# Optimization experiments

Measured on AMD Instinct MI355X. Metric: run time of the kernel, lower is better.

The kernel has to match this reference:

```python
import jax, jax.numpy as jnp
import numpy as np

PATCH = 32          # feature map is PATCH x PATCH, N = PATCH**2 tokens
HEADS = 8
HD = 24             # head_dim (hardcoded in Block -> Cluster3D)
P = 4               # proposal_w = proposal_h = 4 -> 16 cluster centers
EPS_NORM = 1e-12    # F.normalize eps
LN_EPS = 1e-5


def _layernorm(x, g, b):
    m = x.mean(-1, keepdims=True)
    v = ((x - m) ** 2).mean(-1, keepdims=True)
    return (x - m) / jnp.sqrt(v + LN_EPS) * g + b


def _cluster3d(xn, f_w, f_b, v_w, v_b, alpha, beta, proj_w, proj_b):
    # xn: [B, N, D] with tokens laid out row-major over a PATCH x PATCH grid
    B, N, D = xn.shape
    M = P * P
    feat = xn @ f_w.T + f_b   # [B, N, HEADS*HD]  (1x1 conv f)
    val = xn @ v_w.T + v_b    # [B, N, HEADS*HD]  (1x1 conv v)

    def to_heads(t):  # channel layout is (e c): head-major
        return t.reshape(B, N, HEADS, HD).transpose(0, 2, 1, 3).reshape(B * HEADS, N, HD)

    fh = to_heads(feat)       # [Bh, N, HD]
    vh = to_heads(val)

    def pool(t):  # AdaptiveAvgPool to (P, P) over the PATCH x PATCH grid
        g = t.reshape(-1, P, PATCH // P, P, PATCH // P, HD).mean(axis=(2, 4))
        return g.reshape(-1, M, HD)

    centers = pool(fh)        # [Bh, M, HD]
    vcenters = pool(vh)       # [Bh, M, HD]

    cn = centers / jnp.clip(jnp.linalg.norm(centers, axis=-1, keepdims=True), EPS_NORM)
    fn = fh / jnp.clip(jnp.linalg.norm(fh, axis=-1, keepdims=True), EPS_NORM)
    sim = beta + alpha * jnp.einsum('bmc,bnc->bmn', cn, fn)   # [Bh, M, N]
    sim = jnp.where(sim >= 0, sim, 0.2 * sim)                 # LeakyReLU(0.2); dropout eval=identity

    # hard top-1 assignment of each token to its best center
    idx = jnp.argmax(sim, axis=1)                              # [Bh, N]
    mask = jax.nn.one_hot(idx, M, dtype=sim.dtype).transpose(0, 2, 1)  # [Bh, M, N]
    mask = jax.lax.stop_gradient(mask)
    sim = sim * mask

    # aggregate tokens into centers, then dispatch back
    agg = (jnp.einsum('bmn,bnc->bmc', sim, vh) + vcenters) / (mask.sum(-1, keepdims=True) + 1.0)
    out = jnp.einsum('bmn,bmc->bnc', sim, agg)                 # [Bh, N, HD]

    out = out.reshape(B, HEADS, N, HD).transpose(0, 2, 1, 3).reshape(B, N, HEADS * HD)
    return out @ proj_w.T + proj_b                             # [B, N, D]


def setup_inputs() -> dict:
    key = jax.random.key(0)
    ks = jax.random.split(key, 8)
    B, N, D, HID, HH = 64, PATCH * PATCH, 512, 2048, HEADS * HD
    s = 0.02
    return {
        'x': jax.random.normal(ks[0], (B, N, D), jnp.float32),
        'ln1_g': jnp.ones((D,), jnp.float32),
        'ln1_b': jnp.zeros((D,), jnp.float32),
        'f_w': jax.random.normal(ks[1], (HH, D), jnp.float32) * s,
        'f_b': jnp.zeros((HH,), jnp.float32),
        'v_w': jax.random.normal(ks[2], (HH, D), jnp.float32) * s,
        'v_b': jnp.zeros((HH,), jnp.float32),
        'sim_alpha': jnp.ones((1,), jnp.float32),
        'sim_beta': jnp.zeros((1,), jnp.float32),
        'proj_w': jax.random.normal(ks[3], (D, HH), jnp.float32) * s,
        'proj_b': jnp.zeros((D,), jnp.float32),
        'ln2_g': jnp.ones((D,), jnp.float32),
        'ln2_b': jnp.zeros((D,), jnp.float32),
        'fc1_w': jax.random.normal(ks[4], (HID, D), jnp.float32) * s,
        'fc1_b': jnp.zeros((HID,), jnp.float32),
        'fc2_w': jax.random.normal(ks[5], (D, HID), jnp.float32) * s,
        'fc2_b': jnp.zeros((D,), jnp.float32),
    }


def reference(x, ln1_g, ln1_b, f_w, f_b, v_w, v_b, sim_alpha, sim_beta,
              proj_w, proj_b, ln2_g, ln2_b, fc1_w, fc1_b, fc2_w, fc2_b):
    x = x + _cluster3d(_layernorm(x, ln1_g, ln1_b), f_w, f_b, v_w, v_b,
                       sim_alpha, sim_beta, proj_w, proj_b)
    h = _layernorm(x, ln2_g, ln2_b)
    h = jax.nn.gelu(h @ fc1_w.T + fc1_b, approximate=False)
    x = x + (h @ fc2_w.T + fc2_b)
    return x
```

## Files before the change

### kernel.cpp

```cpp
#include <hip/hip_runtime.h>


typedef __attribute__((ext_vector_type(8))) short short8;
typedef __attribute__((ext_vector_type(4))) short short4v;
typedef __attribute__((ext_vector_type(4))) float floatx4;

static __device__ __forceinline__ short f2bf(float f) {
  union { float f; unsigned u; } a; a.f = f;
  unsigned r = a.u + 0x7fffu + ((a.u >> 16) & 1u);
  return (short)(r >> 16);
}

static __device__ __forceinline__ void gload_lds16(const short* g, short* l) {
  __builtin_amdgcn_global_load_lds(
      (const __attribute__((address_space(1))) void*)g,
      (__attribute__((address_space(3))) void*)l, 16, 0, 0);
}

__global__ __launch_bounds__(256) void cvt_f32_bf16(
    const float* __restrict__ in, short* __restrict__ out, int n4)
{
  int i = blockIdx.x * 256 + threadIdx.x;
  if (i >= n4) return;
  float4 v = reinterpret_cast<const float4*>(in)[i];
  short4v o;
  o[0] = f2bf(v.x); o[1] = f2bf(v.y); o[2] = f2bf(v.z); o[3] = f2bf(v.w);
  reinterpret_cast<short4v*>(out)[i] = o;
}

__global__ __launch_bounds__(256) void ln_kernel(
    const float* __restrict__ x, const float* __restrict__ g,
    const float* __restrict__ b, short* __restrict__ out)
{
  const int wave = threadIdx.x >> 6, lane = threadIdx.x & 63;
  const size_t row = (size_t)blockIdx.x * 4 + wave;
  const float* xr = x + row * 512;
  const int c = lane * 8;
  float4 v0 = *reinterpret_cast<const float4*>(xr + c);
  float4 v1 = *reinterpret_cast<const float4*>(xr + c + 4);
  float xs[8] = {v0.x, v0.y, v0.z, v0.w, v1.x, v1.y, v1.z, v1.w};
  float s = 0.f, q = 0.f;
#pragma unroll
  for (int k = 0; k < 8; ++k) { s += xs[k]; q += xs[k] * xs[k]; }
#pragma unroll
  for (int off = 32; off; off >>= 1) {
    s += __shfl_xor(s, off);
    q += __shfl_xor(q, off);
  }
  const float mean = s * (1.0f / 512.0f);
  const float var  = q * (1.0f / 512.0f) - mean * mean;
  const float rstd = rsqrtf(var + 1e-5f);
  short8 o;
#pragma unroll
  for (int k = 0; k < 8; ++k)
    o[k] = f2bf((xs[k] - mean) * rstd * g[c + k] + b[c + k]);
  *reinterpret_cast<short8*>(out + row * 512 + c) = o;
}

template<int BM, int BN, int WM, int WN, int EPI>
__global__ __launch_bounds__(256, 2) void gemm_bt(
    const short* __restrict__ A, const short* __restrict__ W,
    const float* __restrict__ bias, const float* __restrict__ resid,
    float* __restrict__ Cf, short* __restrict__ Cb,
    const int N, const int K)
{
  constexpr int BK = 32;
  constexpr int T  = 256;
  constexpr int AC = (BM * BK / 8) / T;
  constexpr int WC = (BN * BK / 8) / T;
  __shared__ short Al[2][BM * BK];
  __shared__ short Wl[2][BN * BK];
  const int tid  = threadIdx.x;
  const int wave = tid >> 6;
  const int lane = tid & 63;
  constexpr int WCOLS = BN / WN;
  const int wm = (wave / WCOLS) * WM;
  const int wn = (wave % WCOLS) * WN;
  constexpr int MI = WM / 16, NJ = WN / 16;
  const int row0 = blockIdx.x * BM;
  const int col0 = blockIdx.y * BN;
  const int r  = lane & 15;
  const int kc = lane >> 4;

  floatx4 acc[MI][NJ];
#pragma unroll
  for (int i = 0; i < MI; ++i)
#pragma unroll
    for (int j = 0; j < NJ; ++j)
      acc[i][j] = (floatx4){0.f, 0.f, 0.f, 0.f};

  const short* Ab = A + (size_t)row0 * K;
  const short* Wb = W + (size_t)col0 * K;

  const short* aSrc[AC]; int aDst[AC];
#pragma unroll
  for (int u = 0; u < AC; ++u) {
    const int cc = u * T + tid;
    const int rr = cc >> 2, sl = cc & 3;
    const int co = sl ^ ((rr >> 1) & 3);
    aSrc[u] = Ab + (size_t)rr * K + co * 8;
    aDst[u] = cc * 8;
  }
  const short* wSrc[WC]; int wDst[WC];
#pragma unroll
  for (int u = 0; u < WC; ++u) {
    const int cc = u * T + tid;
    const int rr = cc >> 2, sl = cc & 3;
    const int co = sl ^ ((rr >> 1) & 3);
    wSrc[u] = Wb + (size_t)rr * K + co * 8;
    wDst[u] = cc * 8;
  }
  int aOff[MI], wOff[NJ];
#pragma unroll
  for (int i = 0; i < MI; ++i) {
    const int rt = wm + 16 * i + r;
    aOff[i] = rt * BK + ((kc ^ ((rt >> 1) & 3)) << 3);
  }
#pragma unroll
  for (int j = 0; j < NJ; ++j) {
    const int rt = wn + 16 * j + r;
    wOff[j] = rt * BK + ((kc ^ ((rt >> 1) & 3)) << 3);
  }

  auto stage = [&](int buf, int k0) {
#pragma unroll
    for (int u = 0; u < AC; ++u) gload_lds16(aSrc[u] + k0, &Al[buf][aDst[u]]);
#pragma unroll
    for (int u = 0; u < WC; ++u) gload_lds16(wSrc[u] + k0, &Wl[buf][wDst[u]]);
  };

  stage(0, 0);
  __syncthreads();
  int cur = 0;
  for (int k0 = BK; k0 <= K; k0 += BK) {
    if (k0 < K) stage(cur ^ 1, k0);
    short8 af[MI], wfr[NJ];
#pragma unroll
    for (int i = 0; i < MI; ++i)
      af[i] = *reinterpret_cast<const short8*>(&Al[cur][aOff[i]]);
#pragma unroll
    for (int j = 0; j < NJ; ++j)
      wfr[j] = *reinterpret_cast<const short8*>(&Wl[cur][wOff[j]]);
#pragma unroll
    for (int i = 0; i < MI; ++i)
#pragma unroll
      for (int j = 0; j < NJ; ++j)
        acc[i][j] = __builtin_amdgcn_mfma_f32_16x16x32_bf16(
            af[i], wfr[j], acc[i][j], 0, 0, 0);
    __syncthreads();
    cur ^= 1;
  }

#pragma unroll
  for (int i = 0; i < MI; ++i) {
#pragma unroll
    for (int j = 0; j < NJ; ++j) {
      const int col = col0 + wn + 16 * j + r;
      const float bv = bias[col];
#pragma unroll
      for (int t = 0; t < 4; ++t) {
        const int rowi = row0 + wm + 16 * i + (lane >> 4) * 4 + t;
        const size_t offo = (size_t)rowi * N + col;
        float v = acc[i][j][t] + bv;
        if (EPI == 0) {
          Cf[offo] = v;
        } else if (EPI == 1) {
          Cf[offo] = v + resid[offo];
        } else {
          v = 0.5f * v * (1.0f + erff(v * 0.70710678118654752f));
          Cb[offo] = f2bf(v);
        }
      }
    }
  }
}

template<int EPI>
__global__ __launch_bounds__(512, 1) void gemm512(
    const short* __restrict__ A, const short* __restrict__ W,
    const float* __restrict__ bias, const float* __restrict__ resid,
    float* __restrict__ Cf, short* __restrict__ Cb,
    const int N, const int K)
{
  constexpr int BM = 256, BN = 256, BK = 32;
  constexpr int T  = 512;
  constexpr int AC = (BM * BK / 8) / T;
  constexpr int WC = (BN * BK / 8) / T;
  constexpr int WM = 128, WN = 64;
  constexpr int MI = WM / 16, NJ = WN / 16;
  __shared__ short Al[2][BM * BK];
  __shared__ short Wl[2][BN * BK];
  const int tid  = threadIdx.x;
  const int wave = tid >> 6;
  const int lane = tid & 63;
  const int wm = (wave >> 2) * WM;
  const int wn = (wave & 3) * WN;
  const int row0 = blockIdx.x * BM;
  const int col0 = blockIdx.y * BN;
  const int r  = lane & 15;
  const int kc = lane >> 4;

  floatx4 acc[MI][NJ];
#pragma unroll
  for (int i = 0; i < MI; ++i)
#pragma unroll
    for (int j = 0; j < NJ; ++j)
      acc[i][j] = (floatx4){0.f, 0.f, 0.f, 0.f};

  const short* Ab = A + (size_t)row0 * K;
  const short* Wb = W + (size_t)col0 * K;

  const short* aSrc[AC]; int aDst[AC];
#pragma unroll
  for (int u = 0; u < AC; ++u) {
    const int cc = u * T + tid;
    const int rr = cc >> 2, sl = cc & 3;
    const int co = sl ^ ((rr >> 1) & 3);
    aSrc[u] = Ab + (size_t)rr * K + co * 8;
    aDst[u] = cc * 8;
  }
  const short* wSrc[WC]; int wDst[WC];
#pragma unroll
  for (int u = 0; u < WC; ++u) {
    const int cc = u * T + tid;
    const int rr = cc >> 2, sl = cc & 3;
    const int co = sl ^ ((rr >> 1) & 3);
    wSrc[u] = Wb + (size_t)rr * K + co * 8;
    wDst[u] = cc * 8;
  }
  int aOff[MI], wOff[NJ];
#pragma unroll
  for (int i = 0; i < MI; ++i) {
    const int rt = wm + 16 * i + r;
    aOff[i] = rt * BK + ((kc ^ ((rt >> 1) & 3)) << 3);
  }
#pragma unroll
  for (int j = 0; j < NJ; ++j) {
    const int rt = wn + 16 * j + r;
    wOff[j] = rt * BK + ((kc ^ ((rt >> 1) & 3)) << 3);
  }

  auto stage = [&](int buf, int k0) {
#pragma unroll
    for (int u = 0; u < AC; ++u) gload_lds16(aSrc[u] + k0, &Al[buf][aDst[u]]);
#pragma unroll
    for (int u = 0; u < WC; ++u) gload_lds16(wSrc[u] + k0, &Wl[buf][wDst[u]]);
  };

  stage(0, 0);
  __syncthreads();
  int cur = 0;
  for (int k0 = BK; k0 <= K; k0 += BK) {
    if (k0 < K) stage(cur ^ 1, k0);
    short8 af[MI], wfr[NJ];
#pragma unroll
    for (int i = 0; i < MI; ++i)
      af[i] = *reinterpret_cast<const short8*>(&Al[cur][aOff[i]]);
#pragma unroll
    for (int j = 0; j < NJ; ++j)
      wfr[j] = *reinterpret_cast<const short8*>(&Wl[cur][wOff[j]]);
#pragma unroll
    for (int i = 0; i < MI; ++i)
#pragma unroll
      for (int j = 0; j < NJ; ++j)
        acc[i][j] = __builtin_amdgcn_mfma_f32_16x16x32_bf16(
            af[i], wfr[j], acc[i][j], 0, 0, 0);
    __syncthreads();
    cur ^= 1;
  }

#pragma unroll
  for (int i = 0; i < MI; ++i) {
#pragma unroll
    for (int j = 0; j < NJ; ++j) {
      const int col = col0 + wn + 16 * j + r;
      const float bv = bias[col];
#pragma unroll
      for (int t = 0; t < 4; ++t) {
        const int rowi = row0 + wm + 16 * i + kc * 4 + t;
        const size_t offo = (size_t)rowi * N + col;
        float v = acc[i][j][t] + bv;
        if (EPI == 1) {
          Cf[offo] = v + resid[offo];
        } else {
          v = 0.5f * v * (1.0f + erff(v * 0.70710678118654752f));
          Cb[offo] = f2bf(v);
        }
      }
    }
  }
}

__global__ __launch_bounds__(384) void pool_kernel(
    const float* __restrict__ feat, const float* __restrict__ val,
    float* __restrict__ cn, float* __restrict__ vcent)
{
  const int bh = blockIdx.x;
  const int b = bh >> 3, h = bh & 7;
  const int t = threadIdx.x;
  const int m = t / 24, c = t % 24;
  const int cy = m >> 2, cx = m & 3;
  const size_t base = (size_t)b * 1024 * 192 + h * 24 + c;
  float sf = 0.f, sv = 0.f;
  for (int dy = 0; dy < 8; ++dy) {
    const int ny = (cy * 8 + dy) * 32 + cx * 8;
    for (int dx = 0; dx < 8; ++dx) {
      const size_t off = base + (size_t)(ny + dx) * 192;
      sf += feat[off];
      sv += val[off];
    }
  }
  sf *= (1.0f / 64.0f); sv *= (1.0f / 64.0f);
  __shared__ float cent[16][24];
  cent[m][c] = sf;
  vcent[(size_t)bh * 384 + t] = sv;
  __syncthreads();
  float nrm = 0.f;
#pragma unroll
  for (int k = 0; k < 24; ++k) nrm += cent[m][k] * cent[m][k];
  nrm = fmaxf(sqrtf(nrm), 1e-12f);
  cn[(size_t)bh * 384 + t] = sf / nrm;
}

__global__ __launch_bounds__(256) void sim_kernel(
    const float* __restrict__ feat, const float* __restrict__ cn,
    const float* __restrict__ alpha_p, const float* __restrict__ beta_p,
    float* __restrict__ sval, int* __restrict__ sidx)
{
  const int bh = blockIdx.y;
  const int b = bh >> 3, h = bh & 7;
  __shared__ float cs[384];
  for (int i = threadIdx.x; i < 384; i += 256) cs[i] = cn[(size_t)bh * 384 + i];
  __syncthreads();
  const int n = blockIdx.x * 256 + threadIdx.x;
  const float* f = feat + (size_t)(b * 1024 + n) * 192 + h * 24;
  float v[24];
#pragma unroll
  for (int k = 0; k < 24; k += 4) {
    float4 t4 = *reinterpret_cast<const float4*>(f + k);
    v[k] = t4.x; v[k + 1] = t4.y; v[k + 2] = t4.z; v[k + 3] = t4.w;
  }
  float q = 0.f;
#pragma unroll
  for (int k = 0; k < 24; ++k) q += v[k] * v[k];
  const float inv = 1.0f / fmaxf(sqrtf(q), 1e-12f);
  const float alpha = alpha_p[0], beta = beta_p[0];
  float best = -3.4e38f; int bi = 0;
#pragma unroll
  for (int m = 0; m < 16; ++m) {
    float d = 0.f;
#pragma unroll
    for (int k = 0; k < 24; ++k) d += cs[m * 24 + k] * v[k];
    float s = beta + alpha * (d * inv);
    s = (s < 0.f) ? 0.2f * s : s;
    if (s > best) { best = s; bi = m; }
  }
  sval[(size_t)bh * 1024 + n] = best;
  sidx[(size_t)bh * 1024 + n] = bi;
}

__global__ __launch_bounds__(256) void agg_kernel(
    const float* __restrict__ val, const float* __restrict__ vcent,
    const float* __restrict__ sval, const int* __restrict__ sidx,
    float* __restrict__ agg)
{
  const int bh = blockIdx.x;
  const int b = bh >> 3, h = bh & 7;
  __shared__ float acc[384];
  __shared__ float cnt[16];
  for (int i = threadIdx.x; i < 384; i += 256) acc[i] = 0.f;
  if (threadIdx.x < 16) cnt[threadIdx.x] = 0.f;
  __syncthreads();
  for (int n = threadIdx.x; n < 1024; n += 256) {
    const float s = sval[(size_t)bh * 1024 + n];
    const int m = sidx[(size_t)bh * 1024 + n];
    atomicAdd(&cnt[m], 1.0f);
    const float* vv = val + (size_t)(b * 1024 + n) * 192 + h * 24;
#pragma unroll
    for (int k = 0; k < 24; ++k) atomicAdd(&acc[m * 24 + k], s * vv[k]);
  }
  __syncthreads();
  for (int i = threadIdx.x; i < 384; i += 256) {
    const int m = i / 24;
    agg[(size_t)bh * 384 + i] = (acc[i] + vcent[(size_t)bh * 384 + i]) / (cnt[m] + 1.0f);
  }
}

__global__ __launch_bounds__(256) void dispatch_kernel(
    const float* __restrict__ sval, const int* __restrict__ sidx,
    const float* __restrict__ agg, short* __restrict__ o)
{
  const int g = blockIdx.x * 256 + threadIdx.x;
  const int h = g & 7, n = (g >> 3) & 1023, b = g >> 13;
  const int bh = b * 8 + h;
  const float s = sval[(size_t)bh * 1024 + n];
  const int m = sidx[(size_t)bh * 1024 + n];
  const float* a = agg + (size_t)bh * 384 + m * 24;
  short* op = o + ((size_t)(b * 1024 + n)) * 192 + h * 24;
  short8 pack[3];
#pragma unroll
  for (int k = 0; k < 24; ++k) pack[k >> 3][k & 7] = f2bf(s * a[k]);
  short8* dst = reinterpret_cast<short8*>(op);
  dst[0] = pack[0]; dst[1] = pack[1]; dst[2] = pack[2];
}

extern "C" void kernel_launch(void* const* d_in, const int* in_sizes, int n_in,
                              void* d_out, int out_size, void* d_ws, size_t ws_size,
                              hipStream_t stream)
{
  const float* x      = (const float*)d_in[0];
  const float* ln1_g  = (const float*)d_in[1];
  const float* ln1_b  = (const float*)d_in[2];
  const float* f_w    = (const float*)d_in[3];
  const float* f_b    = (const float*)d_in[4];
  const float* v_w    = (const float*)d_in[5];
  const float* v_b    = (const float*)d_in[6];
  const float* alpha  = (const float*)d_in[7];
  const float* beta   = (const float*)d_in[8];
  const float* proj_w = (const float*)d_in[9];
  const float* proj_b = (const float*)d_in[10];
  const float* ln2_g  = (const float*)d_in[11];
  const float* ln2_b  = (const float*)d_in[12];
  const float* fc1_w  = (const float*)d_in[13];
  const float* fc1_b  = (const float*)d_in[14];
  const float* fc2_w  = (const float*)d_in[15];
  const float* fc2_b  = (const float*)d_in[16];
  float* out = (float*)d_out;

  char* ws = (char*)d_ws;
  size_t off = 0;
  auto alloc = [&](size_t bytes) -> char* {
    char* p = ws + off;
    off = (off + bytes + 255) & ~(size_t)255;
    return p;
  };
  short* xn   = (short*)alloc(67108864);
  float* feat = (float*)alloc(50331648);
  float* val  = (float*)alloc(50331648);
  short* o    = (short*)alloc(25165824);
  float* x1   = (float*)alloc(134217728);
  short* wf   = (short*)alloc(196608);
  short* wv   = (short*)alloc(196608);
  short* wp   = (short*)alloc(196608);
  short* w1   = (short*)alloc(2097152);
  short* w2   = (short*)alloc(2097152);
  float* cnb  = (float*)alloc(786432);
  float* vcb  = (float*)alloc(786432);
  float* agb  = (float*)alloc(786432);
  float* svb  = (float*)alloc(2097152);
  int*   sib  = (int*)  alloc(2097152);
  short* h  = (short*)feat;

  const size_t h1_bytes = 134217728;
  short* h1;
  int nchunk;
  if (ws_size >= off + h1_bytes) {
    h1 = (short*)alloc(h1_bytes);
    nchunk = 2;
  } else {
    h1 = xn;
    nchunk = 4;
  }
  const int MCH = 65536 / nchunk;

  cvt_f32_bf16<<<96,   256, 0, stream>>>(f_w,    wf, 24576);
  cvt_f32_bf16<<<96,   256, 0, stream>>>(v_w,    wv, 24576);
  cvt_f32_bf16<<<96,   256, 0, stream>>>(proj_w, wp, 24576);
  cvt_f32_bf16<<<1024, 256, 0, stream>>>(fc1_w,  w1, 262144);
  cvt_f32_bf16<<<1024, 256, 0, stream>>>(fc2_w,  w2, 262144);

  ln_kernel<<<16384, 256, 0, stream>>>(x, ln1_g, ln1_b, xn);

  gemm_bt<256, 64, 64, 64, 0><<<dim3(256, 3), 256, 0, stream>>>(
      xn, wf, f_b, nullptr, feat, nullptr, 192, 512);
  gemm_bt<256, 64, 64, 64, 0><<<dim3(256, 3), 256, 0, stream>>>(
      xn, wv, v_b, nullptr, val, nullptr, 192, 512);

  pool_kernel<<<512, 384, 0, stream>>>(feat, val, cnb, vcb);
  sim_kernel<<<dim3(4, 512), 256, 0, stream>>>(feat, cnb, alpha, beta, svb, sib);
  agg_kernel<<<512, 256, 0, stream>>>(val, vcb, svb, sib, agb);
  dispatch_kernel<<<2048, 256, 0, stream>>>(svb, sib, agb, o);

  gemm_bt<128, 128, 64, 64, 1><<<dim3(512, 4), 256, 0, stream>>>(
      o, wp, proj_b, x, x1, nullptr, 512, 192);

  ln_kernel<<<16384, 256, 0, stream>>>(x1, ln2_g, ln2_b, h);

  for (int c = 0; c < nchunk; ++c) {
    const short* hA = h + (size_t)c * MCH * 512;
    gemm512<2><<<dim3(MCH / 256, 8), 512, 0, stream>>>(
        hA, w1, fc1_b, nullptr, nullptr, h1, 2048, 512);
    gemm512<1><<<dim3(MCH / 256, 2), 512, 0, stream>>>(
        h1, w2, fc2_b, x1 + (size_t)c * MCH * 512,
        out + (size_t)c * MCH * 512, nullptr, 512, 2048);
  }
  (void)in_sizes; (void)n_in; (void)out_size;
}
```

Before: 1.184 ms.

## Retune MLP GEMMs for occupancy, fast GELU, and fewer chunks

The MLP GEMM kernel goes from a double-buffered LDS pipeline to a single buffer with launch bounds allowing several blocks per CU. The fc2 GEMM uses a narrower 128-column tile so it launches more blocks. Exact erff is replaced with an Abramowitz-Stegun polynomial erf approximation in the GELU epilogues, and a single-chunk path is added when the workspace is large enough. The aim is more latency hiding through occupancy and cheaper epilogue math, at the cost of giving up load/compute overlap inside a block and a small loss of GELU accuracy.

```diff
diff --git a/kernel.cpp b/kernel.cpp
--- a/kernel.cpp
+++ b/kernel.cpp
@@ -9,6 +9,20 @@
   union { float f; unsigned u; } a; a.f = f;
   unsigned r = a.u + 0x7fffu + ((a.u >> 16) & 1u);
   return (short)(r >> 16);
+}
+
+static __device__ __forceinline__ float gelu_fast(float v) {
+  const float xs = v * 0.70710678118654752f;
+  const float ax = fabsf(xs);
+  const float t  = __frcp_rn(fmaf(0.3275911f, ax, 1.0f));
+  float p = fmaf(t, 1.061405429f, -1.453152027f);
+  p = fmaf(t, p, 1.421413741f);
+  p = fmaf(t, p, -0.284496736f);
+  p = fmaf(t, p, 0.254829592f);
+  p = p * t;
+  const float er = 1.0f - p * __expf(-ax * ax);
+  const float e  = (xs < 0.f) ? -er : er;
+  return 0.5f * v * (1.0f + e);
 }
 
 static __device__ __forceinline__ void gload_lds16(const short* g, short* l) {
@@ -167,36 +181,36 @@
         } else if (EPI == 1) {
           Cf[offo] = v + resid[offo];
         } else {
-          v = 0.5f * v * (1.0f + erff(v * 0.70710678118654752f));
-          Cb[offo] = f2bf(v);
+          Cb[offo] = f2bf(gelu_fast(v));
         }
       }
     }
   }
 }
 
-template<int EPI>
-__global__ __launch_bounds__(512, 1) void gemm512(
+template<int BN_, int WROWS, int EPI>
+__global__ __launch_bounds__(512, 4) void gemm512s(
     const short* __restrict__ A, const short* __restrict__ W,
     const float* __restrict__ bias, const float* __restrict__ resid,
     float* __restrict__ Cf, short* __restrict__ Cb,
     const int N, const int K)
 {
-  constexpr int BM = 256, BN = 256, BK = 32;
+  constexpr int BM = 256, BK = 32;
   constexpr int T  = 512;
   constexpr int AC = (BM * BK / 8) / T;
-  constexpr int WC = (BN * BK / 8) / T;
-  constexpr int WM = 128, WN = 64;
+  constexpr int WC = (BN_ * BK / 8) / T;
+  constexpr int WCOLS = 8 / WROWS;
+  constexpr int WM = BM / WROWS, WN = BN_ / WCOLS;
   constexpr int MI = WM / 16, NJ = WN / 16;
-  __shared__ short Al[2][BM * BK];
-  __shared__ short Wl[2][BN * BK];
+  __shared__ short Al[BM * BK];
+  __shared__ short Wl[BN_ * BK];
   const int tid  = threadIdx.x;
   const int wave = tid >> 6;
   const int lane = tid & 63;
-  const int wm = (wave >> 2) * WM;
-  const int wn = (wave & 3) * WN;
+  const int wm = (wave / WCOLS) * WM;
+  const int wn = (wave % WCOLS) * WN;
   const int row0 = blockIdx.x * BM;
-  const int col0 = blockIdx.y * BN;
+  const int col0 = blockIdx.y * BN_;
   const int r  = lane & 15;
   const int kc = lane >> 4;
 
@@ -240,33 +254,26 @@
     wOff[j] = rt * BK + ((kc ^ ((rt >> 1) & 3)) << 3);
   }
 
-  auto stage = [&](int buf, int k0) {
-#pragma unroll
-    for (int u = 0; u < AC; ++u) gload_lds16(aSrc[u] + k0, &Al[buf][aDst[u]]);
-#pragma unroll
-    for (int u = 0; u < WC; ++u) gload_lds16(wSrc[u] + k0, &Wl[buf][wDst[u]]);
-  };
-
-  stage(0, 0);
-  __syncthreads();
-  int cur = 0;
-  for (int k0 = BK; k0 <= K; k0 += BK) {
-    if (k0 < K) stage(cur ^ 1, k0);
-    short8 af[MI], wfr[NJ];
+  for (int k0 = 0; k0 < K; k0 += BK) {
+#pragma unroll
+    for (int u = 0; u < AC; ++u) gload_lds16(aSrc[u] + k0, &Al[aDst[u]]);
+#pragma unroll
+    for (int u = 0; u < WC; ++u) gload_lds16(wSrc[u] + k0, &Wl[wDst[u]]);
+    __syncthreads();
+    short8 af[MI], wf[NJ];
 #pragma unroll
     for (int i = 0; i < MI; ++i)
-      af[i] = *reinterpret_cast<const short8*>(&Al[cur][aOff[i]]);
+      af[i] = *reinterpret_cast<const short8*>(&Al[aOff[i]]);
 #pragma unroll
     for (int j = 0; j < NJ; ++j)
-      wfr[j] = *reinterpret_cast<const short8*>(&Wl[cur][wOff[j]]);
+      wf[j] = *reinterpret_cast<const short8*>(&Wl[wOff[j]]);
 #pragma unroll
     for (int i = 0; i < MI; ++i)
 #pragma unroll
       for (int j = 0; j < NJ; ++j)
         acc[i][j] = __builtin_amdgcn_mfma_f32_16x16x32_bf16(
-            af[i], wfr[j], acc[i][j], 0, 0, 0);
+            af[i], wf[j], acc[i][j], 0, 0, 0);
     __syncthreads();
-    cur ^= 1;
   }
 
 #pragma unroll
@@ -276,15 +283,14 @@
       const int col = col0 + wn + 16 * j + r;
       const float bv = bias[col];
 #pragma unroll
-      for (int t = 0; t < 4; ++t) {
-        const int rowi = row0 + wm + 16 * i + kc * 4 + t;
+      for (int tt = 0; tt < 4; ++tt) {
+        const int rowi = row0 + wm + 16 * i + kc * 4 + tt;
         const size_t offo = (size_t)rowi * N + col;
-        float v = acc[i][j][t] + bv;
+        float v = acc[i][j][tt] + bv;
         if (EPI == 1) {
           Cf[offo] = v + resid[offo];
         } else {
-          v = 0.5f * v * (1.0f + erff(v * 0.70710678118654752f));
-          Cb[offo] = f2bf(v);
+          Cb[offo] = f2bf(gelu_fast(v));
         }
       }
     }
@@ -451,11 +457,13 @@
   int*   sib  = (int*)  alloc(2097152);
   short* h  = (short*)feat;
 
-  const size_t h1_bytes = 134217728;
   short* h1;
   int nchunk;
-  if (ws_size >= off + h1_bytes) {
-    h1 = (short*)alloc(h1_bytes);
+  if (ws_size >= off + 268435456) {
+    h1 = (short*)alloc(268435456);
+    nchunk = 1;
+  } else if (ws_size >= off + 134217728) {
+    h1 = (short*)alloc(134217728);
     nchunk = 2;
   } else {
     h1 = xn;
@@ -488,11 +496,12 @@
 
   for (int c = 0; c < nchunk; ++c) {
     const short* hA = h + (size_t)c * MCH * 512;
-    gemm512<2><<<dim3(MCH / 256, 8), 512, 0, stream>>>(
+    float* x1c = x1 + (size_t)c * MCH * 512;
+    float* outc = out + (size_t)c * MCH * 512;
+    gemm512s<256, 2, 2><<<dim3(MCH / 256, 8), 512, 0, stream>>>(
         hA, w1, fc1_b, nullptr, nullptr, h1, 2048, 512);
-    gemm512<1><<<dim3(MCH / 256, 2), 512, 0, stream>>>(
-        h1, w2, fc2_b, x1 + (size_t)c * MCH * 512,
-        out + (size_t)c * MCH * 512, nullptr, 512, 2048);
+    gemm512s<128, 4, 1><<<dim3(MCH / 256, 4), 512, 0, stream>>>(
+        h1, w2, fc2_b, x1c, outc, nullptr, 512, 2048);
   }
   (void)in_sizes; (void)n_in; (void)out_size;
 }
```

Result: slower. 1.957 ms (+65.4%).
